# Kernel optimization log

Hardware: AMD Instinct MI355X
Metric: run time of the kernel (lower is better)

The kernel has to match this reference:

```python
import jax, jax.numpy as jnp
import numpy as np

D_MODEL = 1024
N_HEADS = 16
D_K = D_MODEL // N_HEADS
LN_EPS = 1e-5
NEG = -1e9


def setup_inputs() -> dict:
    key = jax.random.key(0)
    ks = jax.random.split(key, 12)
    B, S = 4, 2048
    s = 1.0 / np.sqrt(D_MODEL)
    # causal mask (1 = keep, 0 = masked)
    causal = jnp.tril(jnp.ones((S, S), dtype=jnp.int32))
    mask = jnp.broadcast_to(causal[None, None], (B, 1, S, S))
    return {
        "Q": jax.random.normal(ks[0], (B, S, D_MODEL), jnp.float32),
        "K": jax.random.normal(ks[1], (B, S, D_MODEL), jnp.float32),
        "V": jax.random.normal(ks[2], (B, S, D_MODEL), jnp.float32),
        "mask": mask,
        "Wq": jax.random.normal(ks[3], (D_MODEL, D_MODEL), jnp.float32) * s,
        "bq": jnp.zeros((D_MODEL,), jnp.float32),
        "Wk": jax.random.normal(ks[4], (D_MODEL, D_MODEL), jnp.float32) * s,
        "bk": jnp.zeros((D_MODEL,), jnp.float32),
        "Wv": jax.random.normal(ks[5], (D_MODEL, D_MODEL), jnp.float32) * s,
        "bv": jnp.zeros((D_MODEL,), jnp.float32),
        "Wo": jax.random.normal(ks[6], (D_MODEL, D_MODEL), jnp.float32) * s,
        "bo": jnp.zeros((D_MODEL,), jnp.float32),
        "ln_gamma": jnp.ones((D_MODEL,), jnp.float32),
        "ln_beta": jnp.zeros((D_MODEL,), jnp.float32),
    }


def _split_heads(x, B, S):
    # (B,S,D) -> (B,H,S,d_k)
    return x.reshape(B, S, N_HEADS, D_K).transpose(0, 2, 1, 3)


def reference(Q, K, V, mask, Wq, bq, Wk, bk, Wv, bv, Wo, bo, ln_gamma, ln_beta):
    B, S, _ = Q.shape
    residual = Q
    q = _split_heads(Q @ Wq + bq, B, S)
    k = _split_heads(K @ Wk + bk, B, S)
    v = _split_heads(V @ Wv + bv, B, S)
    scores = jnp.einsum("bhqd,bhkd->bhqk", q, k) / np.sqrt(D_K).astype(np.float32)
    scores = jnp.where(mask == 0, jnp.float32(NEG), scores)
    attn = jax.nn.softmax(scores, axis=-1)  # dropout p=0 -> identity
    ctx = jnp.einsum("bhqk,bhkd->bhqd", attn, v)
    ctx = ctx.transpose(0, 2, 1, 3).reshape(B, S, D_MODEL)
    out = ctx @ Wo + bo
    x = out + residual
    mu = jnp.mean(x, axis=-1, keepdims=True)
    var = jnp.mean(jnp.square(x - mu), axis=-1, keepdims=True)
    y = (x - mu) * jax.lax.rsqrt(var + LN_EPS) * ln_gamma + ln_beta
    return (y, attn)
```

## Files before the change

### kernel.cpp

```cpp
#include <hip/hip_runtime.h>

#define D_MODEL 1024
#define NH 16
#define DKH 64
#define SEQ 2048
#define BATCH 4
#define ROWS (BATCH*SEQ)

typedef _Float16 f16;
typedef _Float16 f16x4 __attribute__((ext_vector_type(4)));
typedef _Float16 f16x8 __attribute__((ext_vector_type(8)));
typedef float f32x4 __attribute__((ext_vector_type(4)));

#define MFMA16(a,b,c) __builtin_amdgcn_mfma_f32_16x16x32_f16((a),(b),(c),0,0,0)
#define CFENCE() asm volatile("" ::: "memory")

__device__ __forceinline__ void gload16(const void* g, void* l) {
  __builtin_amdgcn_global_load_lds((const __attribute__((address_space(1))) void*)g,
                                   (__attribute__((address_space(3))) void*)l,
                                   16, 0, 0);
}


__global__ __launch_bounds__(256) void cvt_w_kernel(const float* __restrict__ Wq,
    const float* __restrict__ Wk, const float* __restrict__ Wv, const float* __restrict__ Wo,
    f16* __restrict__ dst)
{
  const float* W = (blockIdx.z==0)?Wq:(blockIdx.z==1)?Wk:(blockIdx.z==2)?Wv:Wo;
  f16* d = dst + (size_t)blockIdx.z * ((size_t)D_MODEL*D_MODEL);
  int idx = blockIdx.x*256 + threadIdx.x;
  int k = idx>>10, n = idx&1023;
  d[(size_t)n*D_MODEL + k] = (f16)W[idx];
}


template<int AF32>
__global__ __launch_bounds__(256) void gemm128(
    const void* __restrict__ A0, const void* __restrict__ A1, const void* __restrict__ A2,
    const f16* __restrict__ WTbase,
    const float* __restrict__ bias0, const float* __restrict__ bias1, const float* __restrict__ bias2,
    f16* __restrict__ out0, f16* __restrict__ out1, f16* __restrict__ out2,
    const float* __restrict__ resid, float* __restrict__ xout, int modeBase)
{
  __shared__ __align__(128) char ldsb[49152];
  const int t = threadIdx.x, w = t>>6, l = t&63;
  const int nwg = (int)gridDim.x;
  const int wg = ((int)blockIdx.x & 7) * (nwg >> 3) + ((int)blockIdx.x >> 3);
  const int z  = wg >> 9;
  const int r2 = wg & 511;
  const int bm = r2 >> 3, bn = r2 & 7;
  const int mode = modeBase + z;
  const f16* WT = WTbase + (size_t)mode * ((size_t)D_MODEL*D_MODEL);
  const float* bias = (mode==0)?bias0:(mode==1)?bias1:(mode==2)?bias2:bias0;
  const int wm = w>>1, wn = w&1;
  const int lr = l>>2, lc = l&3, fr = l&15, fg = l>>4;
  f32x4 acc[4][4] = {};
  const char* Bb = (const char*)(WT + (size_t)bn*128*D_MODEL);

#define BAR_FENCED() do { __builtin_amdgcn_s_barrier(); CFENCE(); } while(0)

  if constexpr (AF32) {
    const float* A32 = (const float*)((z==0)?A0:(z==1)?A1:A2);
    const char* Ag = (const char*)A32 + ((size_t)(bm*128 + (t>>3)) * 4096)
                     + (size_t)(((t&7) ^ ((t>>3)&7)) << 4);
    const int su0 = (((fg*2)   ^ (fr&7)) << 4);
    const int su1 = (((fg*2+1) ^ (fr&7)) << 4);

#define STAGEA32(bufv, ktv) do { \
    _Pragma("unroll") \
    for (int cc=0; cc<4; ++cc) \
      gload16(Ag + (size_t)cc*131072 + (size_t)(ktv)*128, ldsb + (bufv)*16384 + cc*4096 + t*16); \
  } while(0)

#define STAGEB32(bufv, ktv) do { \
    char* Bd = ldsb + 32768 + (bufv)*8192; \
    _Pragma("unroll") \
    for (int cc=0; cc<2; ++cc) { \
      int r0 = w*32 + cc*16; \
      gload16(Bb + (size_t)(r0+lr)*2048 + (ktv)*64 + lc*16, Bd + r0*64); \
    } \
  } while(0)

#define COMPUTE32(bufv) do { \
    const char* Abl = ldsb + (bufv)*16384; \
    const f16* Bc = (const f16*)(ldsb + 32768 + (bufv)*8192); \
    f16x8 a[4], b[4]; \
    _Pragma("unroll") \
    for (int i=0;i<4;++i) { \
      const char* rb = Abl + (wm*64 + i*16 + fr)*128; \
      f32x4 lo = *(const f32x4*)(rb + su0); \
      f32x4 hi = *(const f32x4*)(rb + su1); \
      f16x8 t8; \
      _Pragma("unroll") \
      for (int m2=0;m2<4;++m2) { t8[m2] = (f16)lo[m2]; t8[4+m2] = (f16)hi[m2]; } \
      a[i] = t8; \
    } \
    _Pragma("unroll") \
    for (int j=0;j<4;++j) b[j] = *(const f16x8*)(Bc + (wn*64+j*16+fr)*32 + fg*8); \
    _Pragma("unroll") \
    for (int i=0;i<4;++i) \
      _Pragma("unroll") \
      for (int j=0;j<4;++j) \
        acc[i][j] = MFMA16(a[i], b[j], acc[i][j]); \
  } while(0)

    STAGEA32(0, 0); STAGEB32(0, 0);
    CFENCE();
    for (int kt=0; kt<31; ++kt) {
      const int cur = kt & 1;
      STAGEA32(cur^1, kt+1);
      STAGEB32(cur^1, kt+1);
      asm volatile("s_waitcnt vmcnt(6)" ::: "memory");
      BAR_FENCED();
      COMPUTE32(cur);
      CFENCE();
      BAR_FENCED();
    }
    asm volatile("s_waitcnt vmcnt(0)" ::: "memory");
    BAR_FENCED();
    COMPUTE32(1);

#undef STAGEA32
#undef STAGEB32
#undef COMPUTE32
  } else {
    const char* Ab = (const char*)((const f16*)A0 + (size_t)bm*128*D_MODEL);

#define STAGE16(bufv, ktv) do { \
    char* Ad = ldsb + (bufv)*8192; \
    char* Bd = ldsb + 24576 + (bufv)*8192; \
    _Pragma("unroll") \
    for (int cc=0; cc<2; ++cc) { \
      int r0 = w*32 + cc*16; \
      gload16(Ab + (size_t)(r0+lr)*2048 + (ktv)*64 + lc*16, Ad + r0*64); \
      gload16(Bb + (size_t)(r0+lr)*2048 + (ktv)*64 + lc*16, Bd + r0*64); \
    } \
  } while(0)

#define COMPUTE16(bufv) do { \
    const f16* Ac = (const f16*)(ldsb + (bufv)*8192); \
    const f16* Bc = (const f16*)(ldsb + 24576 + (bufv)*8192); \
    f16x8 a[4], b[4]; \
    _Pragma("unroll") \
    for (int i=0;i<4;++i) a[i] = *(const f16x8*)(Ac + (wm*64+i*16+fr)*32 + fg*8); \
    _Pragma("unroll") \
    for (int j=0;j<4;++j) b[j] = *(const f16x8*)(Bc + (wn*64+j*16+fr)*32 + fg*8); \
    _Pragma("unroll") \
    for (int i=0;i<4;++i) \
      _Pragma("unroll") \
      for (int j=0;j<4;++j) \
        acc[i][j] = MFMA16(a[i], b[j], acc[i][j]); \
  } while(0)

    STAGE16(0, 0); STAGE16(1, 1);
    CFENCE();
    for (int kt=0; kt<30; ++kt) {
      STAGE16((kt+2)%3, kt+2);
      asm volatile("s_waitcnt vmcnt(8)" ::: "memory");
      BAR_FENCED();
      COMPUTE16(kt%3);
      CFENCE();
      BAR_FENCED();
    }
    asm volatile("s_waitcnt vmcnt(4)" ::: "memory");
    BAR_FENCED();
    COMPUTE16(0);
    CFENCE();
    BAR_FENCED();
    asm volatile("s_waitcnt vmcnt(0)" ::: "memory");
    BAR_FENCED();
    COMPUTE16(1);

#undef STAGE16
#undef COMPUTE16
  }

#undef BAR_FENCED

  #pragma unroll
  for (int j=0;j<4;++j) {
    int col = bn*128 + wn*64 + j*16 + fr;
    float bz = bias[col];
    #pragma unroll
    for (int i=0;i<4;++i) {
      int row0 = bm*128 + wm*64 + i*16 + fg*4;
      f32x4 v = acc[i][j];
      if (mode==0) {
        int hh = col>>6, dk = col&63;
        #pragma unroll
        for (int r=0;r<4;++r) {
          int row = row0+r; int b_ = row>>11, s = row&(SEQ-1);
          out0[((size_t)(b_*NH+hh)*SEQ + s)*DKH + dk] = (f16)((v[r]+bz)*0.125f);
        }
      } else if (mode==1) {
        int hh = col>>6, dk = col&63;
        #pragma unroll
        for (int r=0;r<4;++r) {
          int row = row0+r; int b_ = row>>11, s = row&(SEQ-1);
          out1[((size_t)(b_*NH+hh)*SEQ + s)*DKH + dk] = (f16)(v[r]+bz);
        }
      } else if (mode==2) {
        int hh = col>>6, dk = col&63;
        int b_ = row0>>11, s0 = row0&(SEQ-1);
        f16x4 pk;
        #pragma unroll
        for (int r=0;r<4;++r) pk[r] = (f16)(v[r]+bz);
        *(f16x4*)(out2 + ((size_t)(b_*NH+hh)*DKH + dk)*SEQ + s0) = pk;
      } else {
        #pragma unroll
        for (int r=0;r<4;++r) {
          size_t o = (size_t)(row0+r)*D_MODEL + col;
          xout[o] = v[r] + bz + resid[o];
        }
      }
    }
  }
}


__global__ __launch_bounds__(256) void attn_kernel(
    const f16* __restrict__ qws, const f16* __restrict__ kws, const f16* __restrict__ vTws,
    float* __restrict__ attn, f16* __restrict__ ctx)
{
  __shared__ f16 el[4][32*128];
  const int t = threadIdx.x, w = t>>6, l = t&63;
  const int wg = ((int)blockIdx.x & 7)*64 + ((int)blockIdx.x >> 3);
  const int bh = wg >> 3;
  const int pr = wg & 7;
  const int qtA = pr, qtB = 15 - pr;
  const int fr = l & 15, fg = l >> 4;
  const f16* kp = kws + (size_t)bh*SEQ*DKH;
  const f16* vp = vTws + (size_t)bh*DKH*SEQ;
  const f16* qpA = qws + ((size_t)bh*SEQ + (size_t)qtA*128)*DKH;
  const f16* qpB = qws + ((size_t)bh*SEQ + (size_t)qtB*128)*DKH;
  float* apA = attn + ((size_t)bh*SEQ + (size_t)qtA*128)*SEQ;
  float* apB = attn + ((size_t)bh*SEQ + (size_t)qtB*128)*SEQ;
  f16* elw = (f16*)&el[w][0];
  const int swzx = (fr & 7) << 2;
  const int rbrow = l >> 5;
  const int rbslot = l & 31;

  f16x8 qfA[2][2], qfB[2][2];
  #pragma unroll
  for (int i=0;i<2;++i)
    #pragma unroll
    for (int kc=0;kc<2;++kc) {
      qfA[i][kc] = *(const f16x8*)(qpA + (w*32 + i*16 + fr)*DKH + kc*32 + fg*8);
      qfB[i][kc] = *(const f16x8*)(qpB + (w*32 + i*16 + fr)*DKH + kc*32 + fg*8);
    }

  auto fill_tile = [&](float* apr, int kt2) {
    f32x4 z4 = {0.f,0.f,0.f,0.f};
    #pragma unroll
    for (int i2=0;i2<16;++i2) {
      int idx = t + i2*256;
      int row = idx >> 5, c4 = idx & 31;
      __builtin_nontemporal_store(z4, (f32x4*)(apr + (size_t)row*SEQ + (size_t)kt2*128 + c4*4));
    }
  };
  const int cB = pr;

  float psumA[2] = {0.f,0.f}, psumB[2] = {0.f,0.f};
  int u = 0, f = 0;
  const int np1 = qtB + 1;
  auto drip_fills = [&]() {
    while (f*np1 < u*15) {
      if (f < cB) fill_tile(apB, qtB+1+f);
      else        fill_tile(apA, qtA+1+(f-cB));
      ++f;
    }
  };

  for (int kt=0; kt<=qtA; ++kt) {
    const f16* kb = kp + (size_t)kt*128*DKH;
    const bool diagA = (kt == qtA);
    #pragma unroll
    for (int jh=0; jh<2; ++jh) {
      f32x4 scB[2][4] = {};
      f32x4 scA[2][4] = {};
      #pragma unroll
      for (int j2=0;j2<4;++j2) {
        const int j = jh*4 + j2;
        #pragma unroll
        for (int kc=0;kc<2;++kc) {
          f16x8 kf = *(const f16x8*)(kb + (j*16+fr)*DKH + kc*32 + fg*8);
          scB[0][j2] = MFMA16(kf, qfB[0][kc], scB[0][j2]);
          scB[1][j2] = MFMA16(kf, qfB[1][kc], scB[1][j2]);
          scA[0][j2] = MFMA16(kf, qfA[0][kc], scA[0][j2]);
          scA[1][j2] = MFMA16(kf, qfA[1][kc], scA[1][j2]);
        }
      }
      #pragma unroll
      for (int i=0;i<2;++i)
        #pragma unroll
        for (int j2=0;j2<4;++j2)
          #pragma unroll
          for (int r=0;r<4;++r) psumB[i] += __expf(scB[i][j2][r]);
      if (diagA) {
        #pragma unroll
        for (int i=0;i<2;++i) {
          int rloc = w*32 + i*16 + fr;
          #pragma unroll
          for (int j2=0;j2<4;++j2)
            #pragma unroll
            for (int r=0;r<4;++r) {
              int cloc = (jh*4+j2)*16 + fg*4 + r;
              if (cloc <= rloc) psumA[i] += __expf(scA[i][j2][r]);
            }
        }
      } else {
        #pragma unroll
        for (int i=0;i<2;++i)
          #pragma unroll
          for (int j2=0;j2<4;++j2)
            #pragma unroll
            for (int r=0;r<4;++r) psumA[i] += __expf(scA[i][j2][r]);
      }
    }
    ++u; drip_fills();
  }

  for (int kt=qtA+1; kt<=qtB; ++kt) {
    const f16* kb = kp + (size_t)kt*128*DKH;
    const bool diagB = (kt == qtB);
    #pragma unroll
    for (int jh=0; jh<2; ++jh) {
      f32x4 sc[2][4] = {};
      #pragma unroll
      for (int j2=0;j2<4;++j2) {
        const int j = jh*4 + j2;
        #pragma unroll
        for (int kc=0;kc<2;++kc) {
          f16x8 kf = *(const f16x8*)(kb + (j*16+fr)*DKH + kc*32 + fg*8);
          sc[0][j2] = MFMA16(kf, qfB[0][kc], sc[0][j2]);
          sc[1][j2] = MFMA16(kf, qfB[1][kc], sc[1][j2]);
        }
      }
      if (diagB) {
        #pragma unroll
        for (int i=0;i<2;++i) {
          int rloc = w*32 + i*16 + fr;
          #pragma unroll
          for (int j2=0;j2<4;++j2)
            #pragma unroll
            for (int r=0;r<4;++r) {
              int cloc = (jh*4+j2)*16 + fg*4 + r;
              if (cloc <= rloc) psumB[i] += __expf(sc[i][j2][r]);
            }
        }
      } else {
        #pragma unroll
        for (int i=0;i<2;++i)
          #pragma unroll
          for (int j2=0;j2<4;++j2)
            #pragma unroll
            for (int r=0;r<4;++r) psumB[i] += __expf(sc[i][j2][r]);
      }
    }
    ++u; drip_fills();
  }

  #pragma unroll
  for (int m=16; m<64; m<<=1) {
    psumA[0] += __shfl_xor(psumA[0], m, 64);
    psumA[1] += __shfl_xor(psumA[1], m, 64);
    psumB[0] += __shfl_xor(psumB[0], m, 64);
    psumB[1] += __shfl_xor(psumB[1], m, 64);
  }
  float rinvA[2] = {1.f/psumA[0], 1.f/psumA[1]};
  float rinvB[2] = {1.f/psumB[0], 1.f/psumB[1]};

  f32x4 av[2][4];
  auto pass2_tile = [&](int ktv, bool diag, const f16x8 (&qf)[2][2], const float (&rinv)[2], float* apr) {
    const f16* kb = kp + (size_t)ktv*128*DKH;
    #pragma unroll
    for (int jh=0; jh<2; ++jh) {
      f32x4 sc[2][4] = {};
      __builtin_amdgcn_s_setprio(1);
      #pragma unroll
      for (int j2=0;j2<4;++j2) {
        const int j = jh*4 + j2;
        #pragma unroll
        for (int kc=0;kc<2;++kc) {
          f16x8 kf = *(const f16x8*)(kb + (j*16+fr)*DKH + kc*32 + fg*8);
          sc[0][j2] = MFMA16(kf, qf[0][kc], sc[0][j2]);
          sc[1][j2] = MFMA16(kf, qf[1][kc], sc[1][j2]);
        }
      }
      __builtin_amdgcn_s_setprio(0);
      #pragma unroll
      for (int i=0;i<2;++i) {
        const int rloc = w*32 + i*16 + fr;
        #pragma unroll
        for (int j2=0;j2<4;++j2) {
          const int j = jh*4 + j2;
          f16x4 ef;
          #pragma unroll
          for (int r=0;r<4;++r) {
            int cloc = j*16 + fg*4 + r;
            float e = (diag && cloc > rloc) ? 0.f : __expf(sc[i][j2][r]) * rinv[i];
            ef[r] = (f16)e;
          }
          *(f16x4*)(elw + (i*16+fr)*128 + (((j*4+fg) ^ swzx) << 2)) = ef;
        }
      }
    }
    __builtin_amdgcn_s_setprio(1);
    #pragma unroll
    for (int c=0;c<4;++c) {
      f16x8 pf0 = *(const f16x8*)(elw + (fr)*128    + (((c*8+fg*2) ^ swzx) << 2));
      f16x8 pf1 = *(const f16x8*)(elw + (16+fr)*128 + (((c*8+fg*2) ^ swzx) << 2));
      #pragma unroll
      for (int j2=0;j2<4;++j2) {
        f16x8 vf = *(const f16x8*)(vp + (j2*16+fr)*SEQ + ktv*128 + c*32 + fg*8);
        av[0][j2] = MFMA16(vf, pf0, av[0][j2]);
        av[1][j2] = MFMA16(vf, pf1, av[1][j2]);
      }
    }
    __builtin_amdgcn_s_setprio(0);
    {
      float* apk = apr + (size_t)(w*32)*SEQ + (size_t)ktv*128;
      #pragma unroll
      for (int p=0;p<16;++p) {
        int row = p*2 + rbrow;
        f16x4 pv4 = *(const f16x4*)(elw + row*128 + ((rbslot ^ ((row&7)<<2)) << 2));
        f32x4 o4; o4[0]=(float)pv4[0]; o4[1]=(float)pv4[1]; o4[2]=(float)pv4[2]; o4[3]=(float)pv4[3];
        __builtin_nontemporal_store(o4, (f32x4*)(apk + (size_t)row*SEQ + rbslot*4));
      }
    }
  };
  auto ctx_store = [&](int qtv) {
    const int b_ = bh >> 4, hh = bh & 15;
    #pragma unroll
    for (int i=0;i<2;++i) {
      size_t rowoff = ((size_t)b_*SEQ + (size_t)qtv*128 + w*32 + i*16 + fr) * D_MODEL + hh*DKH;
      #pragma unroll
      for (int j2=0;j2<4;++j2) {
        f16x4 pk;
        #pragma unroll
        for (int r=0;r<4;++r) pk[r] = (f16)av[i][j2][r];
        *(f16x4*)(ctx + rowoff + j2*16 + fg*4) = pk;
      }
    }
  };

  #pragma unroll
  for (int i=0;i<2;++i)
    #pragma unroll
    for (int j2=0;j2<4;++j2) av[i][j2] = (f32x4){0.f,0.f,0.f,0.f};
  for (int kt=0; kt<=qtA; ++kt) pass2_tile(kt, kt==qtA, qfA, rinvA, apA);
  ctx_store(qtA);

  #pragma unroll
  for (int i=0;i<2;++i)
    #pragma unroll
    for (int j2=0;j2<4;++j2) av[i][j2] = (f32x4){0.f,0.f,0.f,0.f};
  for (int kt=0; kt<=qtB; ++kt) pass2_tile(kt, kt==qtB, qfB, rinvB, apB);
  ctx_store(qtB);
}


__global__ __launch_bounds__(256) void ln_kernel(const float* __restrict__ x,
    const float* __restrict__ gamma, const float* __restrict__ beta, float* __restrict__ y)
{
  __shared__ float red[4];
  __shared__ float red2[4];
  const int t = threadIdx.x, w = t>>6, l = t&63;
  const size_t row = blockIdx.x;
  float4 v = ((const float4*)(x + row*D_MODEL))[t];
  float s = v.x+v.y+v.z+v.w;
  #pragma unroll
  for (int m=1;m<64;m<<=1) s += __shfl_xor(s, m, 64);
  if (l==0) red[w] = s;
  __syncthreads();
  float mu = (red[0]+red[1]+red[2]+red[3]) * (1.f/D_MODEL);
  float dx=v.x-mu, dy=v.y-mu, dz=v.z-mu, dw=v.w-mu;
  float q = dx*dx+dy*dy+dz*dz+dw*dw;
  #pragma unroll
  for (int m=1;m<64;m<<=1) q += __shfl_xor(q, m, 64);
  if (l==0) red2[w] = q;
  __syncthreads();
  float var = (red2[0]+red2[1]+red2[2]+red2[3]) * (1.f/D_MODEL);
  float rs = rsqrtf(var + 1e-5f);
  float4 g  = ((const float4*)gamma)[t];
  float4 bb = ((const float4*)beta)[t];
  float4 o;
  o.x = dx*rs*g.x + bb.x;
  o.y = dy*rs*g.y + bb.y;
  o.z = dz*rs*g.z + bb.z;
  o.w = dw*rs*g.w + bb.w;
  ((float4*)(y + row*D_MODEL))[t] = o;
}


extern "C" void kernel_launch(void* const* d_in, const int* in_sizes, int n_in,
                              void* d_out, int out_size, void* d_ws, size_t ws_size,
                              hipStream_t stream)
{
  const float* Q  = (const float*)d_in[0];
  const float* K  = (const float*)d_in[1];
  const float* V  = (const float*)d_in[2];
  const float* Wq = (const float*)d_in[4];
  const float* bq = (const float*)d_in[5];
  const float* Wk = (const float*)d_in[6];
  const float* bk = (const float*)d_in[7];
  const float* Wv = (const float*)d_in[8];
  const float* bv = (const float*)d_in[9];
  const float* Wo = (const float*)d_in[10];
  const float* bo = (const float*)d_in[11];
  const float* gam= (const float*)d_in[12];
  const float* bet= (const float*)d_in[13];

  float* y    = (float*)d_out;
  float* attn = y + (size_t)ROWS*D_MODEL;

  char* ws = (char*)d_ws;
  const size_t SZ = (size_t)ROWS*D_MODEL*sizeof(f16);
  f16* ctx   = (f16*)ws;
  float* xb  = (float*)(ws + SZ);
  f16* WT    = (f16*)(ws + 3*SZ);
  f16* qws   = (f16*)(ws + 3*SZ + ((size_t)4*D_MODEL*D_MODEL*sizeof(f16)));
  f16* kws   = (f16*)((char*)qws + SZ);
  f16* vT    = (f16*)((char*)kws + SZ);

  cvt_w_kernel<<<dim3(4096,1,4), 256, 0, stream>>>(Wq, Wk, Wv, Wo, WT);
  gemm128<1><<<1536, 256, 0, stream>>>(Q, K, V, WT, bq, bk, bv, qws, kws, vT, nullptr, nullptr, 0);
  attn_kernel<<<512, 256, 0, stream>>>(qws, kws, vT, attn, ctx);
  gemm128<0><<<512, 256, 0, stream>>>(ctx, nullptr, nullptr, WT, bo, bo, bo, nullptr, nullptr, nullptr, Q, xb, 3);
  ln_kernel<<<8192, 256, 0, stream>>>(xb, gam, bet, y);
}
```

Measured before the change: 455.9 us.

## Split paired query tiles across two wave groups in 512-thread attention blocks

The attention kernel now launches 512 threads per block. Each group of four waves handles one of the two paired query tiles (pr and 15-pr), where before a single set of four waves processed both tiles in sequence. This removes the shared-K pass-1 loop and the serial second pass, so both tiles are computed concurrently. In exchange, pass 1 loads K separately for each tile, LDS use doubles, and the two groups have unequal work (qt+1 tiles each), so waves in the short group sit idle. Zero-fill of masked tiles is spread per group in proportion to its compute loop.

```diff
diff --git a/kernel.cpp b/kernel.cpp
--- a/kernel.cpp
+++ b/kernel.cpp
@@ -218,94 +218,76 @@
 }
 
 
-__global__ __launch_bounds__(256) void attn_kernel(
+__global__ __launch_bounds__(512, 2) void attn_kernel(
     const f16* __restrict__ qws, const f16* __restrict__ kws, const f16* __restrict__ vTws,
     float* __restrict__ attn, f16* __restrict__ ctx)
 {
-  __shared__ f16 el[4][32*128];
+  __shared__ f16 el[8][32*128];
   const int t = threadIdx.x, w = t>>6, l = t&63;
   const int wg = ((int)blockIdx.x & 7)*64 + ((int)blockIdx.x >> 3);
   const int bh = wg >> 3;
   const int pr = wg & 7;
-  const int qtA = pr, qtB = 15 - pr;
+  const int grp = w >> 2;
+  const int wl = w & 3;
+  const int qt = grp ? (15 - pr) : pr;
   const int fr = l & 15, fg = l >> 4;
   const f16* kp = kws + (size_t)bh*SEQ*DKH;
   const f16* vp = vTws + (size_t)bh*DKH*SEQ;
-  const f16* qpA = qws + ((size_t)bh*SEQ + (size_t)qtA*128)*DKH;
-  const f16* qpB = qws + ((size_t)bh*SEQ + (size_t)qtB*128)*DKH;
-  float* apA = attn + ((size_t)bh*SEQ + (size_t)qtA*128)*SEQ;
-  float* apB = attn + ((size_t)bh*SEQ + (size_t)qtB*128)*SEQ;
+  const f16* qp = qws + ((size_t)bh*SEQ + (size_t)qt*128)*DKH;
+  float* ap = attn + ((size_t)bh*SEQ + (size_t)qt*128)*SEQ;
   f16* elw = (f16*)&el[w][0];
   const int swzx = (fr & 7) << 2;
   const int rbrow = l >> 5;
   const int rbslot = l & 31;
-
-  f16x8 qfA[2][2], qfB[2][2];
+  const int tg = wl*64 + l;
+
+  f16x8 qf[2][2];
   #pragma unroll
   for (int i=0;i<2;++i)
     #pragma unroll
-    for (int kc=0;kc<2;++kc) {
-      qfA[i][kc] = *(const f16x8*)(qpA + (w*32 + i*16 + fr)*DKH + kc*32 + fg*8);
-      qfB[i][kc] = *(const f16x8*)(qpB + (w*32 + i*16 + fr)*DKH + kc*32 + fg*8);
-    }
-
-  auto fill_tile = [&](float* apr, int kt2) {
+    for (int kc=0;kc<2;++kc)
+      qf[i][kc] = *(const f16x8*)(qp + (wl*32 + i*16 + fr)*DKH + kc*32 + fg*8);
+
+  auto fill_tile = [&](int kt2) {
     f32x4 z4 = {0.f,0.f,0.f,0.f};
     #pragma unroll
     for (int i2=0;i2<16;++i2) {
-      int idx = t + i2*256;
+      int idx = tg + i2*256;
       int row = idx >> 5, c4 = idx & 31;
-      __builtin_nontemporal_store(z4, (f32x4*)(apr + (size_t)row*SEQ + (size_t)kt2*128 + c4*4));
+      __builtin_nontemporal_store(z4, (f32x4*)(ap + (size_t)row*SEQ + (size_t)kt2*128 + c4*4));
     }
   };
-  const int cB = pr;
-
-  float psumA[2] = {0.f,0.f}, psumB[2] = {0.f,0.f};
-  int u = 0, f = 0;
-  const int np1 = qtB + 1;
-  auto drip_fills = [&]() {
-    while (f*np1 < u*15) {
-      if (f < cB) fill_tile(apB, qtB+1+f);
-      else        fill_tile(apA, qtA+1+(f-cB));
-      ++f;
-    }
-  };
-
-  for (int kt=0; kt<=qtA; ++kt) {
+  const int nComp = qt + 1;
+  const int nFill = 15 - qt;
+
+  float psum[2] = {0.f, 0.f};
+  int f = 0;
+  for (int kt=0; kt<=qt; ++kt) {
     const f16* kb = kp + (size_t)kt*128*DKH;
-    const bool diagA = (kt == qtA);
+    const bool diag = (kt == qt);
     #pragma unroll
     for (int jh=0; jh<2; ++jh) {
-      f32x4 scB[2][4] = {};
-      f32x4 scA[2][4] = {};
+      f32x4 sc[2][4] = {};
       #pragma unroll
       for (int j2=0;j2<4;++j2) {
         const int j = jh*4 + j2;
         #pragma unroll
         for (int kc=0;kc<2;++kc) {
           f16x8 kf = *(const f16x8*)(kb + (j*16+fr)*DKH + kc*32 + fg*8);
-          scB[0][j2] = MFMA16(kf, qfB[0][kc], scB[0][j2]);
-          scB[1][j2] = MFMA16(kf, qfB[1][kc], scB[1][j2]);
-          scA[0][j2] = MFMA16(kf, qfA[0][kc], scA[0][j2]);
-          scA[1][j2] = MFMA16(kf, qfA[1][kc], scA[1][j2]);
-        }
-      }
-      #pragma unroll
-      for (int i=0;i<2;++i)
-        #pragma unroll
-        for (int j2=0;j2<4;++j2)
-          #pragma unroll
-          for (int r=0;r<4;++r) psumB[i] += __expf(scB[i][j2][r]);
-      if (diagA) {
+          sc[0][j2] = MFMA16(kf, qf[0][kc], sc[0][j2]);
+          sc[1][j2] = MFMA16(kf, qf[1][kc], sc[1][j2]);
+        }
+      }
+      if (diag) {
         #pragma unroll
         for (int i=0;i<2;++i) {
-          int rloc = w*32 + i*16 + fr;
+          int rloc = wl*32 + i*16 + fr;
           #pragma unroll
           for (int j2=0;j2<4;++j2)
             #pragma unroll
             for (int r=0;r<4;++r) {
               int cloc = (jh*4+j2)*16 + fg*4 + r;
-              if (cloc <= rloc) psumA[i] += __expf(scA[i][j2][r]);
+              if (cloc <= rloc) psum[i] += __expf(sc[i][j2][r]);
             }
         }
       } else {
@@ -314,65 +296,29 @@
           #pragma unroll
           for (int j2=0;j2<4;++j2)
             #pragma unroll
-            for (int r=0;r<4;++r) psumA[i] += __expf(scA[i][j2][r]);
-      }
-    }
-    ++u; drip_fills();
-  }
-
-  for (int kt=qtA+1; kt<=qtB; ++kt) {
+            for (int r=0;r<4;++r) psum[i] += __expf(sc[i][j2][r]);
+      }
+    }
+    while (f*nComp < (kt+1)*nFill) { fill_tile(qt+1+f); ++f; }
+  }
+  while (f < nFill) { fill_tile(qt+1+f); ++f; }
+
+  #pragma unroll
+  for (int m=16; m<64; m<<=1) {
+    psum[0] += __shfl_xor(psum[0], m, 64);
+    psum[1] += __shfl_xor(psum[1], m, 64);
+  }
+  float rinv[2] = {1.f/psum[0], 1.f/psum[1]};
+
+  f32x4 av[2][4];
+  #pragma unroll
+  for (int i=0;i<2;++i)
+    #pragma unroll
+    for (int j2=0;j2<4;++j2) av[i][j2] = (f32x4){0.f,0.f,0.f,0.f};
+
+  for (int kt=0; kt<=qt; ++kt) {
     const f16* kb = kp + (size_t)kt*128*DKH;
-    const bool diagB = (kt == qtB);
-    #pragma unroll
-    for (int jh=0; jh<2; ++jh) {
-      f32x4 sc[2][4] = {};
-      #pragma unroll
-      for (int j2=0;j2<4;++j2) {
-        const int j = jh*4 + j2;
-        #pragma unroll
-        for (int kc=0;kc<2;++kc) {
-          f16x8 kf = *(const f16x8*)(kb + (j*16+fr)*DKH + kc*32 + fg*8);
-          sc[0][j2] = MFMA16(kf, qfB[0][kc], sc[0][j2]);
-          sc[1][j2] = MFMA16(kf, qfB[1][kc], sc[1][j2]);
-        }
-      }
-      if (diagB) {
-        #pragma unroll
-        for (int i=0;i<2;++i) {
-          int rloc = w*32 + i*16 + fr;
-          #pragma unroll
-          for (int j2=0;j2<4;++j2)
-            #pragma unroll
-            for (int r=0;r<4;++r) {
-              int cloc = (jh*4+j2)*16 + fg*4 + r;
-              if (cloc <= rloc) psumB[i] += __expf(sc[i][j2][r]);
-            }
-        }
-      } else {
-        #pragma unroll
-        for (int i=0;i<2;++i)
-          #pragma unroll
-          for (int j2=0;j2<4;++j2)
-            #pragma unroll
-            for (int r=0;r<4;++r) psumB[i] += __expf(sc[i][j2][r]);
-      }
-    }
-    ++u; drip_fills();
-  }
-
-  #pragma unroll
-  for (int m=16; m<64; m<<=1) {
-    psumA[0] += __shfl_xor(psumA[0], m, 64);
-    psumA[1] += __shfl_xor(psumA[1], m, 64);
-    psumB[0] += __shfl_xor(psumB[0], m, 64);
-    psumB[1] += __shfl_xor(psumB[1], m, 64);
-  }
-  float rinvA[2] = {1.f/psumA[0], 1.f/psumA[1]};
-  float rinvB[2] = {1.f/psumB[0], 1.f/psumB[1]};
-
-  f32x4 av[2][4];
-  auto pass2_tile = [&](int ktv, bool diag, const f16x8 (&qf)[2][2], const float (&rinv)[2], float* apr) {
-    const f16* kb = kp + (size_t)ktv*128*DKH;
+    const bool diag = (kt == qt);
     #pragma unroll
     for (int jh=0; jh<2; ++jh) {
       f32x4 sc[2][4] = {};
@@ -390,7 +336,7 @@
       __builtin_amdgcn_s_setprio(0);
       #pragma unroll
       for (int i=0;i<2;++i) {
-        const int rloc = w*32 + i*16 + fr;
+        const int rloc = wl*32 + i*16 + fr;
         #pragma unroll
         for (int j2=0;j2<4;++j2) {
           const int j = jh*4 + j2;
@@ -412,14 +358,14 @@
       f16x8 pf1 = *(const f16x8*)(elw + (16+fr)*128 + (((c*8+fg*2) ^ swzx) << 2));
       #pragma unroll
       for (int j2=0;j2<4;++j2) {
-        f16x8 vf = *(const f16x8*)(vp + (j2*16+fr)*SEQ + ktv*128 + c*32 + fg*8);
+        f16x8 vf = *(const f16x8*)(vp + (j2*16+fr)*SEQ + kt*128 + c*32 + fg*8);
         av[0][j2] = MFMA16(vf, pf0, av[0][j2]);
         av[1][j2] = MFMA16(vf, pf1, av[1][j2]);
       }
     }
     __builtin_amdgcn_s_setprio(0);
     {
-      float* apk = apr + (size_t)(w*32)*SEQ + (size_t)ktv*128;
+      float* apk = ap + (size_t)(wl*32)*SEQ + (size_t)kt*128;
       #pragma unroll
       for (int p=0;p<16;++p) {
         int row = p*2 + rbrow;
@@ -428,12 +374,13 @@
         __builtin_nontemporal_store(o4, (f32x4*)(apk + (size_t)row*SEQ + rbslot*4));
       }
     }
-  };
-  auto ctx_store = [&](int qtv) {
+  }
+
+  {
     const int b_ = bh >> 4, hh = bh & 15;
     #pragma unroll
     for (int i=0;i<2;++i) {
-      size_t rowoff = ((size_t)b_*SEQ + (size_t)qtv*128 + w*32 + i*16 + fr) * D_MODEL + hh*DKH;
+      size_t rowoff = ((size_t)b_*SEQ + (size_t)qt*128 + wl*32 + i*16 + fr) * D_MODEL + hh*DKH;
       #pragma unroll
       for (int j2=0;j2<4;++j2) {
         f16x4 pk;
@@ -442,21 +389,7 @@
         *(f16x4*)(ctx + rowoff + j2*16 + fg*4) = pk;
       }
     }
-  };
-
-  #pragma unroll
-  for (int i=0;i<2;++i)
-    #pragma unroll
-    for (int j2=0;j2<4;++j2) av[i][j2] = (f32x4){0.f,0.f,0.f,0.f};
-  for (int kt=0; kt<=qtA; ++kt) pass2_tile(kt, kt==qtA, qfA, rinvA, apA);
-  ctx_store(qtA);
-
-  #pragma unroll
-  for (int i=0;i<2;++i)
-    #pragma unroll
-    for (int j2=0;j2<4;++j2) av[i][j2] = (f32x4){0.f,0.f,0.f,0.f};
-  for (int kt=0; kt<=qtB; ++kt) pass2_tile(kt, kt==qtB, qfB, rinvB, apB);
-  ctx_store(qtB);
+  }
 }
 
 
@@ -525,7 +458,7 @@
 
   cvt_w_kernel<<<dim3(4096,1,4), 256, 0, stream>>>(Wq, Wk, Wv, Wo, WT);
   gemm128<1><<<1536, 256, 0, stream>>>(Q, K, V, WT, bq, bk, bv, qws, kws, vT, nullptr, nullptr, 0);
-  attn_kernel<<<512, 256, 0, stream>>>(qws, kws, vT, attn, ctx);
+  attn_kernel<<<512, 512, 0, stream>>>(qws, kws, vT, attn, ctx);
   gemm128<0><<<512, 256, 0, stream>>>(ctx, nullptr, nullptr, WT, bo, bo, bo, nullptr, nullptr, nullptr, Q, xb, 3);
   ln_kernel<<<8192, 256, 0, stream>>>(xb, gam, bet, y);
 }
```

Result: faster. 427.6 us (median of 2 runs) (-6.2%).
